# Optimization experiments

Hardware: AMD Instinct MI355X
Metric: run time of the kernel (lower is better)

Reference implementation:

```python
import jax, jax.numpy as jnp
import numpy as np

V_TEXT = 256
V_TOTAL = 4352
B, H, TQ, TK = 8, 4, 800, 128
T_TOK = 1024
BLANK_LOGPROB = -8.0
NEG = -1e9  # finite stand-in for -inf (keeps grads nan-free)
CE_W = 1.5
ATTN_W = 10.0
ATTN_START = 5000


def setup_inputs() -> dict:
    key = jax.random.key(0)
    ks = jax.random.split(key, 6)
    logits = jax.random.normal(ks[0], (B, T_TOK, V_TOTAL), dtype=jnp.float32)
    attn_logprob = jax.random.normal(ks[1], (B, H, TQ, TK), dtype=jnp.float32)
    token_targets = jax.random.randint(ks[2], (B, T_TOK), V_TEXT, V_TOTAL, dtype=jnp.int32)
    audio_target_lens = jax.random.randint(ks[3], (B,), 512, T_TOK + 1, dtype=jnp.int32)
    src_lens = jax.random.randint(ks[4], (B,), 64, TK + 1, dtype=jnp.int32)  # key (text) lens
    out_lens = jax.random.randint(ks[5], (B,), 400, TQ + 1, dtype=jnp.int32)  # query (audio) lens
    return {"logits": logits, "attn_logprob": attn_logprob, "token_targets": token_targets,
            "audio_target_lens": audio_target_lens, "src_lens": src_lens, "out_lens": out_lens,
            "current_step": 6000}


def _masked_ce(logits, targets, valid_mask):
    # CE over the audio slice of the shared vocab; pads ignored; divide by mask count.
    v_audio = logits.shape[-1] - V_TEXT
    logp = jax.nn.log_softmax(logits[:, :, V_TEXT:], axis=-1)  # (B,T,Va)
    tgt = targets - V_TEXT
    valid = valid_mask & (targets != -100)
    safe = jnp.clip(tgt, 0, v_audio - 1)
    nll = -jnp.take_along_axis(logp, safe[..., None], axis=-1)[..., 0]  # (B,T)
    loss_sum = jnp.sum(jnp.where(valid, nll, 0.0))
    denom = jnp.maximum(jnp.sum(valid_mask), 1).astype(logp.dtype)
    return loss_sum / denom


def _forward_sum(attn_logprob, key_lens, query_lens):
    # Batched CTC forward-sum over all (batch, head) pairs.
    # Targets for item b are 1..K_b (all distinct), blank = class 0 (padded logit -8).
    Bb, Hh, Tq, Tk = attn_logprob.shape
    N = Bb * Hh
    lp = jnp.pad(attn_logprob, ((0, 0), (0, 0), (0, 0), (1, 0)), constant_values=BLANK_LOGPROB)
    lp = lp.reshape(N, Tq, Tk + 1)
    klens = jnp.repeat(key_lens, Hh)    # (N,)
    qlens = jnp.repeat(query_lens, Hh)  # (N,)
    # masked log_softmax over the first K_b+1 classes only (matches per-item slice)
    cls_valid = jnp.arange(Tk + 1)[None, None, :] < (klens[:, None, None] + 1)
    logp = jax.nn.log_softmax(jnp.where(cls_valid, lp, NEG), axis=-1)  # (N,Tq,Tk+1)

    S = 2 * Tk + 1
    s = jnp.arange(S)
    ext_label = jnp.where(s % 2 == 1, (s + 1) // 2, 0)       # blank,1,blank,2,...
    skip_ok = (s % 2 == 1) & (s >= 2)                        # labels distinct -> skip always ok
    ext_valid = s[None, :] < (2 * klens[:, None] + 1)        # (N,S)
    emit = logp[:, :, ext_label]                             # (N,Tq,S)

    alpha0 = jnp.full((N, S), NEG, dtype=logp.dtype)
    alpha0 = alpha0.at[:, 0].set(emit[:, 0, 0]).at[:, 1].set(emit[:, 0, 1])
    alpha0 = jnp.where(ext_valid, alpha0, NEG)

    def step(alpha, emit_t):
        sh1 = jnp.pad(alpha, ((0, 0), (1, 0)), constant_values=NEG)[:, :-1]
        sh2 = jnp.pad(alpha, ((0, 0), (2, 0)), constant_values=NEG)[:, :-2]
        sh2 = jnp.where(skip_ok[None, :], sh2, NEG)
        a = jnp.logaddexp(jnp.logaddexp(alpha, sh1), sh2) + emit_t
        a = jnp.where(ext_valid, a, NEG)
        return a, a

    _, alphas = jax.lax.scan(step, alpha0, jnp.moveaxis(emit[:, 1:], 1, 0))  # (Tq-1,N,S)
    alphas = jnp.concatenate([alpha0[None], alphas], axis=0)                 # (Tq,N,S)

    alpha_T = alphas[qlens - 1, jnp.arange(N)]  # (N,S) alpha at t = query_len-1
    e1 = jnp.take_along_axis(alpha_T, (2 * klens - 1)[:, None], axis=1)[:, 0]
    e2 = jnp.take_along_axis(alpha_T, (2 * klens)[:, None], axis=1)[:, 0]
    nll = -jnp.logaddexp(e1, e2)
    loss = nll / klens.astype(logp.dtype)  # torch CTCLoss 'mean' divides by target len
    loss = jnp.where(jnp.isfinite(loss) & (loss < 1e8), loss, 0.0)  # zero_infinity
    return jnp.mean(loss)  # == sum_b/B then sum_h/H of the original loops


def _losses(logits, attn_logprob, token_targets, audio_target_lens, src_lens, out_lens, current_step):
    t_tok = token_targets.shape[1]
    valid = jnp.arange(t_tok)[None, :] < audio_target_lens[:, None]
    token_loss = _masked_ce(logits, token_targets, valid)
    if current_step > ATTN_START:
        q = jnp.minimum(out_lens, attn_logprob.shape[2])
        k = jnp.minimum(src_lens, attn_logprob.shape[3])
        attn_loss = _forward_sum(attn_logprob, k, q)
    else:
        attn_loss = jnp.zeros((), dtype=logits.dtype)
    total = token_loss * CE_W + attn_loss * ATTN_W
    return jnp.stack([total, attn_loss, token_loss])


def reference(logits, attn_logprob, token_targets, audio_target_lens, src_lens, out_lens, current_step):
    return _losses(logits, attn_logprob, token_targets, audio_target_lens, src_lens, out_lens, current_step)
```

## Files before the change

### kernel.cpp

```cpp
#include <hip/hip_runtime.h>
#include <hip/hip_bf16.h>
#include <cstdint>
#include <cstddef>

#define V_TEXT   256
#define V_TOTAL  4352
#define V_AUDIO  4096
#define B_       8
#define H_       4
#define TQ_      800
#define TK_      128
#define T_TOK    1024
#define NSEQ     32
#define K2       1.4426950408889634f
#define LN2      0.6931471805599453f
#define EB8      11.541560327111707f
#define EM8      3.3546262790251185e-04f
#define FNEGINF  (-3.0e38f)
#define CHK      30

template <int CTRL>
__device__ __forceinline__ float dpp_mov(float x, float old) {
    return __int_as_float(__builtin_amdgcn_update_dpp(
        __float_as_int(old), __float_as_int(x), CTRL, 0xf, 0xf, false));
}
__device__ __forceinline__ float dpp_shr1_old(float x, float old) {
    return dpp_mov<0x138>(x, old);
}
__device__ __forceinline__ float lane_bcast(float x, int lane) {
    return __int_as_float(__builtin_amdgcn_readlane(__float_as_int(x), lane));
}
__device__ __forceinline__ float wave_max(float x) {
    x = fmaxf(x, dpp_mov<0x111>(x, FNEGINF));
    x = fmaxf(x, dpp_mov<0x112>(x, FNEGINF));
    x = fmaxf(x, dpp_mov<0x114>(x, FNEGINF));
    x = fmaxf(x, dpp_mov<0x118>(x, FNEGINF));
    x = fmaxf(x, dpp_mov<0x142>(x, FNEGINF));
    x = fmaxf(x, dpp_mov<0x143>(x, FNEGINF));
    return lane_bcast(x, 63);
}

__device__ __forceinline__ void stage_rows3(
    float* db, const float* __restrict__ abase, int g0, int pw, int k, int q,
    int lane, float& prod, int& acc)
{
    int half = lane >> 5, col = (lane & 31) * 4;
    int i0 = pw * 5;
    float4 v[5];
    #pragma unroll
    for (int u = 0; u < 5; u++) {
        int rc = min(g0 + 2 * (i0 + u) + half, TQ_ - 1);
        v[u] = *reinterpret_cast<const float4*>(abase + (size_t)rc * TK_ + col);
    }
    #pragma unroll
    for (int u = 0; u < 5; u++) {
        int r  = 2 * (i0 + u) + half;
        int rg = g0 + r;
        float e0 = (col + 0 < k) ? __builtin_exp2f(v[u].x * K2) : 0.0f;
        float e1 = (col + 1 < k) ? __builtin_exp2f(v[u].y * K2) : 0.0f;
        float e2 = (col + 2 < k) ? __builtin_exp2f(v[u].z * K2) : 0.0f;
        float e3 = (col + 3 < k) ? __builtin_exp2f(v[u].w * K2) : 0.0f;
        *reinterpret_cast<float4*>(db + r * TK_ + col) = make_float4(e0, e1, e2, e3);

        float ps = (e0 + e1) + (e2 + e3);
        ps += dpp_mov<0x111>(ps, 0.0f);
        ps += dpp_mov<0x112>(ps, 0.0f);
        ps += dpp_mov<0x114>(ps, 0.0f);
        ps += dpp_mov<0x118>(ps, 0.0f);
        ps += dpp_mov<0x142>(ps, 0.0f);
        ps += EM8;
        prod *= (rg < q) ? ps : 1.0f;
        if (u & 1) {
            int b = __float_as_int(prod);
            acc += (b >> 23) - 127;
            prod = __int_as_float((b & 0x007fffff) | 0x3f800000);
        }
    }
}

__global__ __launch_bounds__(256) void fused_kernel(
    const float* __restrict__ logits, const int* __restrict__ targets,
    const int* __restrict__ alens,
    const float* __restrict__ attn, const int* __restrict__ slens,
    const int* __restrict__ olens,
    float* __restrict__ nll_out, float* __restrict__ loss_out)
{
    __shared__ float buf[2][CHK][TK_];
    __shared__ float cshp[4];

    int tid = threadIdx.x;
    int wid = tid >> 6, lane = tid & 63;

    if (blockIdx.x >= NSEQ) {
        int row = (blockIdx.x - NSEQ) * 4 + wid;
        const float* p = logits + (size_t)row * V_TOTAL + V_TEXT;

        float4 v0 = *reinterpret_cast<const float4*>(p + lane * 4);
        float4 v1 = *reinterpret_cast<const float4*>(p + lane * 4 + 1024);
        float4 v2 = *reinterpret_cast<const float4*>(p + lane * 4 + 2048);
        float4 v3 = *reinterpret_cast<const float4*>(p + lane * 4 + 3072);
        int tg = targets[row];

        float m = fmaxf(fmaxf(fmaxf(v0.x, v0.y), fmaxf(v0.z, v0.w)),
                        fmaxf(fmaxf(v1.x, v1.y), fmaxf(v1.z, v1.w)));
        m = fmaxf(m, fmaxf(fmaxf(v2.x, v2.y), fmaxf(v2.z, v2.w)));
        m = fmaxf(m, fmaxf(fmaxf(v3.x, v3.y), fmaxf(v3.z, v3.w)));
        m = wave_max(m);

        float mn = -m * K2;
        float s =
          __builtin_exp2f(__builtin_fmaf(v0.x,K2,mn)) + __builtin_exp2f(__builtin_fmaf(v0.y,K2,mn))
        + __builtin_exp2f(__builtin_fmaf(v0.z,K2,mn)) + __builtin_exp2f(__builtin_fmaf(v0.w,K2,mn))
        + __builtin_exp2f(__builtin_fmaf(v1.x,K2,mn)) + __builtin_exp2f(__builtin_fmaf(v1.y,K2,mn))
        + __builtin_exp2f(__builtin_fmaf(v1.z,K2,mn)) + __builtin_exp2f(__builtin_fmaf(v1.w,K2,mn))
        + __builtin_exp2f(__builtin_fmaf(v2.x,K2,mn)) + __builtin_exp2f(__builtin_fmaf(v2.y,K2,mn))
        + __builtin_exp2f(__builtin_fmaf(v2.z,K2,mn)) + __builtin_exp2f(__builtin_fmaf(v2.w,K2,mn))
        + __builtin_exp2f(__builtin_fmaf(v3.x,K2,mn)) + __builtin_exp2f(__builtin_fmaf(v3.y,K2,mn))
        + __builtin_exp2f(__builtin_fmaf(v3.z,K2,mn)) + __builtin_exp2f(__builtin_fmaf(v3.w,K2,mn));
        s += dpp_mov<0x111>(s, 0.0f);
        s += dpp_mov<0x112>(s, 0.0f);
        s += dpp_mov<0x114>(s, 0.0f);
        s += dpp_mov<0x118>(s, 0.0f);
        s += dpp_mov<0x142>(s, 0.0f);
        s  = lane_bcast(s, 31) + lane_bcast(s, 63);

        if (lane == 0) {
            float lse = m + __builtin_log2f(s) * LN2;
            int b = row >> 10, t = row & (T_TOK - 1);
            bool valid = (t < alens[b]) && (tg != -100);
            float nll = 0.0f;
            if (valid) {
                int idx = min(max(tg - V_TEXT, 0), V_AUDIO - 1);
                nll = lse - p[idx];
            }
            nll_out[row] = nll;
        }
        return;
    }

    int n = blockIdx.x;
    int k = min(slens[n >> 2], TK_);
    int q = min(olens[n >> 2], TQ_);
    int ncha = (q + CHK - 1) / CHK;
    const float* abase = attn + (size_t)n * TQ_ * TK_;

    float prod = 1.0f;
    int   acc  = 0;

    float p0 = (wid == 0 && lane == 0) ? 1.0f : 0.0f;
    float p1 = 0.0f, p2 = 0.0f, p3 = 0.0f, p4 = 0.0f, p3s = 0.0f;
    int   Mtot = 0;
    int   rsc  = 0;

    if (wid > 0) stage_rows3(&buf[0][0][0], abase, 0, wid - 1, k, q, lane, prod, acc);
    __syncthreads();

#define SSTEP(xv)                                                            \
    do {                                                                     \
        float c01 = p0 + p3s;                                                \
        float c12 = p2 + p1;                                                 \
        float n4  = (p4 + p3) * EM8;                                         \
        p0 = c01 * EM8;                                                      \
        p1 = (p1 + c01) * xv.x;                                              \
        p2 = c12 * EM8;                                                      \
        p3 = (p3 + c12) * xv.y;                                              \
        p4 = n4;                                                             \
        p3s = dpp_shr1_old(p3, 0.0f);                                        \
    } while (0)

#define RESCALE()                                                            \
    do {                                                                     \
        float wm = fmaxf(fmaxf(fmaxf(p0, p1), fmaxf(p2, p3)),                \
                         fmaxf(p4, p3s));                                    \
        wm = wave_max(wm);                                                   \
        int ebits = __float_as_int(wm) & 0x7f800000;                         \
        if (ebits > 0) {                      \
            int se = 274 - (ebits >> 23);              \
            se = se < 1 ? 1 : (se > 254 ? 254 : se);                         \
            float sc = __int_as_float(se << 23);                             \
            Mtot += 127 - se;                                                \
            p0 *= sc; p1 *= sc; p2 *= sc; p3 *= sc; p4 *= sc; p3s *= sc;     \
        }                                                                    \
    } while (0)

    for (int c = 0; c < ncha; c++) {
        if (wid > 0) {
            if (c + 1 < ncha)
                stage_rows3(&buf[(c + 1) & 1][0][0], abase, (c + 1) * CHK,
                            wid - 1, k, q, lane, prod, acc);
        } else {
            const float* lb = &buf[c & 1][0][2 * lane];
            int lim = min(CHK, q - c * CHK);
            int ts = 0;
            if (ts < lim) {
#define LD(j) (*reinterpret_cast<const float2*>(lb + min((j), CHK - 1) * TK_))
                float2 A = LD(0), Bv = LD(1), Cv = LD(2), Dv = LD(3);
                for (; ts + 4 <= lim; ts += 4) {
                    float2 nA = LD(ts + 4), nB = LD(ts + 5),
                           nC = LD(ts + 6), nD = LD(ts + 7);
                    SSTEP(A); SSTEP(Bv); SSTEP(Cv); SSTEP(Dv);
                    if (++rsc == 2) { rsc = 0; RESCALE(); }
                    A = nA; Bv = nB; Cv = nC; Dv = nD;
                }
                for (; ts < lim; ts++) { SSTEP(A); A = Bv; Bv = Cv; Cv = Dv; }
#undef LD
            }
        }
        __syncthreads();
    }
#undef SSTEP
#undef RESCALE

    if (wid > 0) {
        float cl = __builtin_log2f(prod) + (float)acc;
        float cs = lane_bcast(cl, 31) + lane_bcast(cl, 63);
        if (lane == 0) cshp[wid] = cs;
    }
    __syncthreads();

    if (wid == 0) {
        float csh = cshp[1] + cshp[2] + cshp[3];
        int s1 = 2 * k - 1, s2 = 2 * k;
        float e1v, e2v;
        {
            int l = s1 >> 2, r = s1 & 3;
            float c1 = __shfl(p1, l), c3 = __shfl(p3, l);
            e1v = (r == 1) ? c1 : c3;
        }
        if (s2 == 256) {
            e2v = __shfl(p4, 63);
        } else {
            int l = s2 >> 2, r = s2 & 3;
            float c0 = __shfl(p0, l), c2 = __shfl(p2, l);
            e2v = (r == 0) ? c0 : c2;
        }
        float l2 = __builtin_log2f(e1v + e2v) + (float)Mtot - csh;
        float nll = -l2 * LN2;
        float loss = nll / (float)k;
        if (!(isfinite(loss) && loss < 1.0e8f)) loss = 0.0f;
        if (lane == 0) loss_out[n] = loss;
    }
}

__global__ __launch_bounds__(256) void fin_kernel(
    const float* __restrict__ nll, const int* __restrict__ alens,
    const int* __restrict__ step, const float* __restrict__ attn_losses,
    float* __restrict__ out)
{
    __shared__ float red[4];
    int tid = threadIdx.x;
    float s = 0.0f;
    for (int i = tid; i < B_ * T_TOK; i += 256) s += nll[i];
    #pragma unroll
    for (int off = 32; off > 0; off >>= 1) s += __shfl_xor(s, off);
    if ((tid & 63) == 0) red[tid >> 6] = s;
    __syncthreads();
    if (tid == 0) {
        float ce_sum = red[0] + red[1] + red[2] + red[3];
        int denom = 0;
        for (int b = 0; b < B_; b++) denom += min(alens[b], T_TOK);
        denom = max(denom, 1);
        float token = ce_sum / (float)denom;
        float a = 0.0f;
        for (int i = 0; i < NSEQ; i++) a += attn_losses[i];
        a *= (1.0f / NSEQ);
        if (step[0] <= 5000) a = 0.0f;
        out[0] = 1.5f * token + 10.0f * a;
        out[1] = a;
        out[2] = token;
    }
}

extern "C" void kernel_launch(void* const* d_in, const int* in_sizes, int n_in,
                              void* d_out, int out_size, void* d_ws, size_t ws_size,
                              hipStream_t stream)
{
    const float* logits  = (const float*)d_in[0];
    const float* attn    = (const float*)d_in[1];
    const int*   targets = (const int*)d_in[2];
    const int*   alens   = (const int*)d_in[3];
    const int*   slens   = (const int*)d_in[4];
    const int*   olens   = (const int*)d_in[5];
    const int*   step    = (const int*)d_in[6];
    float* out = (float*)d_out;
    float* ws  = (float*)d_ws;

    float* ws_attn = ws;
    float* ws_nll  = ws + 64;

    fused_kernel<<<dim3(NSEQ + B_ * T_TOK / 4), dim3(256), 0, stream>>>(
        logits, targets, alens, attn, slens, olens, ws_nll, ws_attn);
    fin_kernel<<<dim3(1), dim3(256), 0, stream>>>(ws_nll, alens, step, ws_attn, out);
}
```

Before: 238.0 us.

## Deepen attention staging pipeline with register prefetch and triple-buffered LDS chunks

The producer waves now hold two chunks of attention rows in registers (R0/R1) and issue global loads three chunks ahead, writing exp'd values into a triple-buffered shared chunk of 32 rows instead of a double-buffered chunk of 30. The consumer wave processes 8 recurrence steps per group with prefetched LDS reads, overlapping the wave-max rescale reduction with the steps. The rescale exponent target is adjusted to suit the longer interval between rescales. This aims to hide global load latency behind the serial CTC recurrence, at the cost of more registers and LDS per block and a sixth row load per producer wave that is only counted by one wave.

```diff
diff --git a/kernel.cpp b/kernel.cpp
--- a/kernel.cpp
+++ b/kernel.cpp
@@ -1,5 +1,4 @@
 #include <hip/hip_runtime.h>
-#include <hip/hip_bf16.h>
 #include <cstdint>
 #include <cstddef>
 
@@ -7,17 +6,16 @@
 #define V_TOTAL  4352
 #define V_AUDIO  4096
 #define B_       8
-#define H_       4
 #define TQ_      800
 #define TK_      128
 #define T_TOK    1024
 #define NSEQ     32
 #define K2       1.4426950408889634f
 #define LN2      0.6931471805599453f
-#define EB8      11.541560327111707f
 #define EM8      3.3546262790251185e-04f
 #define FNEGINF  (-3.0e38f)
-#define CHK      30
+#define CHK      32
+#define NBUF     3
 
 template <int CTRL>
 __device__ __forceinline__ float dpp_mov(float x, float old) {
@@ -40,20 +38,23 @@
     return lane_bcast(x, 63);
 }
 
-__device__ __forceinline__ void stage_rows3(
-    float* db, const float* __restrict__ abase, int g0, int pw, int k, int q,
-    int lane, float& prod, int& acc)
-{
+__device__ __forceinline__ void load6(float4* v, const float* __restrict__ abase,
+                                      int g0, int pw, int lane) {
     int half = lane >> 5, col = (lane & 31) * 4;
     int i0 = pw * 5;
-    float4 v[5];
     #pragma unroll
-    for (int u = 0; u < 5; u++) {
+    for (int u = 0; u < 6; u++) {
         int rc = min(g0 + 2 * (i0 + u) + half, TQ_ - 1);
         v[u] = *reinterpret_cast<const float4*>(abase + (size_t)rc * TK_ + col);
     }
+}
+
+__device__ __forceinline__ void write6(float* db, const float4* v, int g0, int pw,
+                                       int k, int q, int lane, float& prod, int& acc) {
+    int half = lane >> 5, col = (lane & 31) * 4;
+    int i0 = pw * 5;
     #pragma unroll
-    for (int u = 0; u < 5; u++) {
+    for (int u = 0; u < 6; u++) {
         int r  = 2 * (i0 + u) + half;
         int rg = g0 + r;
         float e0 = (col + 0 < k) ? __builtin_exp2f(v[u].x * K2) : 0.0f;
@@ -69,7 +70,8 @@
         ps += dpp_mov<0x118>(ps, 0.0f);
         ps += dpp_mov<0x142>(ps, 0.0f);
         ps += EM8;
-        prod *= (rg < q) ? ps : 1.0f;
+        bool owned = (u < 5) || (pw == 2);
+        prod *= (owned && rg < q) ? ps : 1.0f;
         if (u & 1) {
             int b = __float_as_int(prod);
             acc += (b >> 23) - 127;
@@ -85,7 +87,7 @@
     const int* __restrict__ olens,
     float* __restrict__ nll_out, float* __restrict__ loss_out)
 {
-    __shared__ float buf[2][CHK][TK_];
+    __shared__ float buf[NBUF][CHK][TK_];
     __shared__ float cshp[4];
 
     int tid = threadIdx.x;
@@ -150,9 +152,15 @@
     float p0 = (wid == 0 && lane == 0) ? 1.0f : 0.0f;
     float p1 = 0.0f, p2 = 0.0f, p3 = 0.0f, p4 = 0.0f, p3s = 0.0f;
     int   Mtot = 0;
-    int   rsc  = 0;
-
-    if (wid > 0) stage_rows3(&buf[0][0][0], abase, 0, wid - 1, k, q, lane, prod, acc);
+
+    float4 R0[6], R1[6];
+
+    if (wid > 0) {
+        load6(R0, abase, 0,       wid - 1, lane);
+        load6(R1, abase, CHK,     wid - 1, lane);
+        write6(&buf[0][0][0], R0, 0, wid - 1, k, q, lane, prod, acc);
+        load6(R0, abase, 2 * CHK, wid - 1, lane);
+    }
     __syncthreads();
 
 #define SSTEP(xv)                                                            \
@@ -168,48 +176,58 @@
         p3s = dpp_shr1_old(p3, 0.0f);                                        \
     } while (0)
 
-#define RESCALE()                                                            \
-    do {                                                                     \
-        float wm = fmaxf(fmaxf(fmaxf(p0, p1), fmaxf(p2, p3)),                \
-                         fmaxf(p4, p3s));                                    \
-        wm = wave_max(wm);                                                   \
-        int ebits = __float_as_int(wm) & 0x7f800000;                         \
-        if (ebits > 0) {                      \
-            int se = 274 - (ebits >> 23);              \
-            se = se < 1 ? 1 : (se > 254 ? 254 : se);                         \
-            float sc = __int_as_float(se << 23);                             \
-            Mtot += 127 - se;                                                \
-            p0 *= sc; p1 *= sc; p2 *= sc; p3 *= sc; p4 *= sc; p3s *= sc;     \
-        }                                                                    \
-    } while (0)
-
     for (int c = 0; c < ncha; c++) {
         if (wid > 0) {
-            if (c + 1 < ncha)
-                stage_rows3(&buf[(c + 1) & 1][0][0], abase, (c + 1) * CHK,
-                            wid - 1, k, q, lane, prod, acc);
+            if (c + 1 < ncha) {
+                float* db = &buf[(c + 1) % NBUF][0][0];
+                if ((c + 1) & 1) write6(db, R1, (c + 1) * CHK, wid - 1, k, q, lane, prod, acc);
+                else             write6(db, R0, (c + 1) * CHK, wid - 1, k, q, lane, prod, acc);
+            }
+            if (c + 3 < ncha) {
+                if ((c + 3) & 1) load6(R1, abase, (c + 3) * CHK, wid - 1, lane);
+                else             load6(R0, abase, (c + 3) * CHK, wid - 1, lane);
+            }
         } else {
-            const float* lb = &buf[c & 1][0][2 * lane];
+            const float* lb = &buf[c % NBUF][0][2 * lane];
             int lim = min(CHK, q - c * CHK);
-            int ts = 0;
-            if (ts < lim) {
-#define LD(j) (*reinterpret_cast<const float2*>(lb + min((j), CHK - 1) * TK_))
-                float2 A = LD(0), Bv = LD(1), Cv = LD(2), Dv = LD(3);
-                for (; ts + 4 <= lim; ts += 4) {
-                    float2 nA = LD(ts + 4), nB = LD(ts + 5),
-                           nC = LD(ts + 6), nD = LD(ts + 7);
-                    SSTEP(A); SSTEP(Bv); SSTEP(Cv); SSTEP(Dv);
-                    if (++rsc == 2) { rsc = 0; RESCALE(); }
-                    A = nA; Bv = nB; Cv = nC; Dv = nD;
+            int nfull = lim >> 3, rem = lim & 7;
+            float2 cur[8], nxt[8];
+            #pragma unroll
+            for (int j = 0; j < 8; j++)
+                cur[j] = *reinterpret_cast<const float2*>(lb + min(j, CHK - 1) * TK_);
+            for (int g = 0; g < nfull; g++) {
+                int base = g * 8;
+                #pragma unroll
+                for (int j = 0; j < 8; j++)
+                    nxt[j] = *reinterpret_cast<const float2*>(lb + min(base + 8 + j, CHK - 1) * TK_);
+                float wm = fmaxf(fmaxf(fmaxf(p0, p1), fmaxf(p2, p3)),
+                                 fmaxf(p4, p3s));
+                #pragma unroll
+                for (int j = 0; j < 8; j++) SSTEP(cur[j]);
+                wm = fmaxf(wm, dpp_mov<0x111>(wm, FNEGINF));
+                wm = fmaxf(wm, dpp_mov<0x112>(wm, FNEGINF));
+                wm = fmaxf(wm, dpp_mov<0x114>(wm, FNEGINF));
+                wm = fmaxf(wm, dpp_mov<0x118>(wm, FNEGINF));
+                wm = fmaxf(wm, dpp_mov<0x142>(wm, FNEGINF));
+                wm = fmaxf(wm, dpp_mov<0x143>(wm, FNEGINF));
+                wm = lane_bcast(wm, 63);
+                int ebits = __float_as_int(wm) & 0x7f800000;
+                if (ebits > 0) {
+                    int se = 222 - (ebits >> 23);
+                    se = se < 1 ? 1 : (se > 254 ? 254 : se);
+                    float sc = __int_as_float(se << 23);
+                    Mtot += 127 - se;
+                    p0 *= sc; p1 *= sc; p2 *= sc; p3 *= sc; p4 *= sc; p3s *= sc;
                 }
-                for (; ts < lim; ts++) { SSTEP(A); A = Bv; Bv = Cv; Cv = Dv; }
-#undef LD
+                #pragma unroll
+                for (int j = 0; j < 8; j++) cur[j] = nxt[j];
             }
+            #pragma unroll
+            for (int j = 0; j < 8; j++) if (j < rem) SSTEP(cur[j]);
         }
         __syncthreads();
     }
 #undef SSTEP
-#undef RESCALE
 
     if (wid > 0) {
         float cl = __builtin_log2f(prod) + (float)acc;
```

Result: no change. 237.0 us (-0.4%).
